# Kernel optimization log

Measured on AMD Instinct MI355X. Metric: run time of the kernel, lower is better.

## Reference

```python
import jax, jax.numpy as jnp
import numpy as np

N = 8_000_000
NUM_MOLS = 200_000

def setup_inputs() -> dict:
    key = jax.random.key(0)
    k1, k2 = jax.random.split(key)
    atoms_x = jax.random.normal(k1, (N, 3), dtype=jnp.float32)
    graph_batch = jnp.sort(jax.random.randint(k2, (N,), 0, NUM_MOLS, dtype=jnp.int64))
    return {"atoms_x": atoms_x, "graph_batch": graph_batch, "num_mols": NUM_MOLS}

def reference(atoms_x, graph_batch, num_mols):
    # Per-molecule mean via single-pass segment reduction (replaces O(N*num_mols) mask loop)
    seg_sum = jax.ops.segment_sum(atoms_x, graph_batch, num_segments=num_mols)          # [M, 3]
    counts = jax.ops.segment_sum(jnp.ones((atoms_x.shape[0],), atoms_x.dtype),
                                 graph_batch, num_segments=num_mols)                    # [M]
    mean = seg_sum / jnp.maximum(counts, 1.0)[:, None]                                  # empty mols -> 0 center
    return atoms_x - mean[graph_batch]
```

## Files before the change

### kernel.cpp

```cpp
#include <hip/hip_runtime.h>


static constexpr int WAVE   = 64;
static constexpr int TPB    = 64;
static constexpr int CPT    = 8;
static constexpr int WCHUNK = WAVE * CPT;
static constexpr int SLOTS  = 96;
static constexpr int NGRP   = WCHUNK / 16;
static constexpr int XGRP   = 216;
static constexpr int IGRP   = 72;

#define LDS_FENCE() asm volatile("s_waitcnt lgkmcnt(0)" ::: "memory")

__device__ void serial_fallback(const float* __restrict__ x,
                                const int* __restrict__ gb,
                                float* __restrict__ out, int n,
                                long long cs, long long ce, int lane) {
  if (lane != 0) return;
  long long i = cs;
  while (i < ce) {
    int id = gb[i];
    long long rs = i; while (rs > 0 && gb[rs - 1] == id) --rs;
    long long re = i; while (re < n && gb[re] == id) ++re;
    float sx = 0.f, sy = 0.f, sz = 0.f;
    for (long long k = rs; k < re; ++k) {
      sx += x[k * 3 + 0]; sy += x[k * 3 + 1]; sz += x[k * 3 + 2];
    }
    float inv = 1.f / (float)(re - rs);
    float mx = sx * inv, my = sy * inv, mz = sz * inv;
    long long we = (re < ce) ? re : ce;
    for (long long k = i; k < we; ++k) {
      out[k * 3 + 0] = x[k * 3 + 0] - mx;
      out[k * 3 + 1] = x[k * 3 + 1] - my;
      out[k * 3 + 2] = x[k * 3 + 2] - mz;
    }
    i = we;
  }
}

__global__ __launch_bounds__(TPB) void fused_center_kernel(
    const float* __restrict__ x, const int* __restrict__ gb,
    float* __restrict__ out, int n) {
  __shared__ alignas(16) char xbuf[NGRP * XGRP];
  __shared__ alignas(16) char ibuf[NGRP * IGRP];
  __shared__ alignas(16) float sums[SLOTS * 4];

  const int lane = threadIdx.x;
  const long long cs = (long long)blockIdx.x * WCHUNK;
  const long long ce = (cs + WCHUNK < (long long)n) ? cs + WCHUNK : (long long)n;

  if (ce - cs < WCHUNK) {
    const int fid = gb[cs];
    const int lid = gb[ce - 1];
    const int span = lid - fid + 1;
    if (span > SLOTS) { serial_fallback(x, gb, out, n, cs, ce, lane); return; }
    for (int s = lane; s < span * 4; s += WAVE) sums[s] = 0.f;
    LDS_FENCE();
    for (long long i = cs + lane; i < ce; i += WAVE) {
      int s = (gb[i] - fid) * 4;
      atomicAdd(&sums[s + 0], x[i * 3 + 0]);
      atomicAdd(&sums[s + 1], x[i * 3 + 1]);
      atomicAdd(&sums[s + 2], x[i * 3 + 2]);
      atomicAdd(&sums[s + 3], 1.f);
    }
    if (cs > 0) {
      float hx = 0.f, hy = 0.f, hz = 0.f, hc = 0.f;
      long long off = 1 + lane;
      for (;;) {
        long long i = cs - off;
        bool m = (i >= 0) && (gb[i] == fid);
        if (m) { hx += x[i*3+0]; hy += x[i*3+1]; hz += x[i*3+2]; hc += 1.f; }
        if (__popcll(__ballot(m)) < WAVE) break;
        off += WAVE;
      }
#pragma unroll
      for (int d = 1; d < 64; d <<= 1) {
        hx += __shfl_xor(hx, d); hy += __shfl_xor(hy, d);
        hz += __shfl_xor(hz, d); hc += __shfl_xor(hc, d);
      }
      if (lane == 0 && hc > 0.f) {
        atomicAdd(&sums[0], hx); atomicAdd(&sums[1], hy);
        atomicAdd(&sums[2], hz); atomicAdd(&sums[3], hc);
      }
    }
    LDS_FENCE();
    for (int s = lane; s < span; s += WAVE) {
      float c = sums[s * 4 + 3];
      if (c > 0.f) {
        float inv = 1.f / c;
        sums[s*4+0] *= inv; sums[s*4+1] *= inv; sums[s*4+2] *= inv;
      }
    }
    LDS_FENCE();
    for (long long i = cs + lane; i < ce; i += WAVE) {
      int s = (gb[i] - fid) * 4;
      out[i * 3 + 0] = x[i * 3 + 0] - sums[s + 0];
      out[i * 3 + 1] = x[i * 3 + 1] - sums[s + 1];
      out[i * 3 + 2] = x[i * 3 + 2] - sums[s + 2];
    }
    return;
  }

  float4 xr[6];
  const float4* xv = reinterpret_cast<const float4*>(x + cs * 3);
#pragma unroll
  for (int j = 0; j < 6; ++j) xr[j] = xv[j * WAVE + lane];
  int4 gr[2];
  const int4* gv = reinterpret_cast<const int4*>(gb + cs);
#pragma unroll
  for (int j = 0; j < 2; ++j) gr[j] = gv[j * WAVE + lane];

#pragma unroll
  for (int j = 0; j < 6; ++j) {
    int i = j * WAVE + lane;
    int k0 = 2 * i, k1 = 2 * i + 1;
    *reinterpret_cast<float2*>(xbuf + (k0 / 24) * XGRP + (k0 % 24) * 8) =
        make_float2(xr[j].x, xr[j].y);
    *reinterpret_cast<float2*>(xbuf + (k1 / 24) * XGRP + (k1 % 24) * 8) =
        make_float2(xr[j].z, xr[j].w);
  }
#pragma unroll
  for (int j = 0; j < 2; ++j) {
    int i = j * WAVE + lane;
    int k0 = 2 * i, k1 = 2 * i + 1;
    *reinterpret_cast<int2*>(ibuf + (k0 / 8) * IGRP + (k0 % 8) * 8) =
        make_int2(gr[j].x, gr[j].y);
    *reinterpret_cast<int2*>(ibuf + (k1 / 8) * IGRP + (k1 % 8) * 8) =
        make_int2(gr[j].z, gr[j].w);
  }
  {
    float4 z = make_float4(0.f, 0.f, 0.f, 0.f);
    reinterpret_cast<float4*>(sums)[lane] = z;
    if (lane < SLOTS - WAVE) reinterpret_cast<float4*>(sums)[WAVE + lane] = z;
  }
  LDS_FENCE();

  int idk[CPT];
  const int a0 = lane * CPT;
#pragma unroll
  for (int j = 0; j < CPT; ++j) {
    int a = a0 + j;
    idk[j] = *reinterpret_cast<const int*>(ibuf + (a / 16) * IGRP + (a % 16) * 4);
  }
  const int fid = __shfl(idk[0], 0);
  const int lid = __shfl(idk[CPT - 1], WAVE - 1);
  const int span = lid - fid + 1;
  if (span > SLOTS) { serial_fallback(x, gb, out, n, cs, ce, lane); return; }

  {
    int cur = idk[0];
    float sx = 0.f, sy = 0.f, sz = 0.f, sc = 0.f;
#pragma unroll
    for (int j = 0; j < CPT; ++j) {
      if (idk[j] != cur) {
        int s = (cur - fid) * 4;
        atomicAdd(&sums[s + 0], sx); atomicAdd(&sums[s + 1], sy);
        atomicAdd(&sums[s + 2], sz); atomicAdd(&sums[s + 3], sc);
        cur = idk[j]; sx = sy = sz = sc = 0.f;
      }
      int a = a0 + j;
      const char* p = xbuf + (a / 16) * XGRP + (a % 16) * 12;
      sx += *reinterpret_cast<const float*>(p + 0);
      sy += *reinterpret_cast<const float*>(p + 4);
      sz += *reinterpret_cast<const float*>(p + 8);
      sc += 1.f;
    }
    int s = (cur - fid) * 4;
    atomicAdd(&sums[s + 0], sx); atomicAdd(&sums[s + 1], sy);
    atomicAdd(&sums[s + 2], sz); atomicAdd(&sums[s + 3], sc);
  }

  if (cs > 0) {
    float hx = 0.f, hy = 0.f, hz = 0.f, hc = 0.f;
    long long off = 1 + lane;
    for (;;) {
      long long i = cs - off;
      bool m = (i >= 0) && (gb[i] == fid);
      if (m) { hx += x[i*3+0]; hy += x[i*3+1]; hz += x[i*3+2]; hc += 1.f; }
      if (__popcll(__ballot(m)) < WAVE) break;
      off += WAVE;
    }
#pragma unroll
    for (int d = 1; d < 64; d <<= 1) {
      hx += __shfl_xor(hx, d); hy += __shfl_xor(hy, d);
      hz += __shfl_xor(hz, d); hc += __shfl_xor(hc, d);
    }
    if (lane == 0 && hc > 0.f) {
      atomicAdd(&sums[0], hx); atomicAdd(&sums[1], hy);
      atomicAdd(&sums[2], hz); atomicAdd(&sums[3], hc);
    }
  }
  if (ce < (long long)n) {
    float hx = 0.f, hy = 0.f, hz = 0.f, hc = 0.f;
    long long off = (long long)lane;
    for (;;) {
      long long i = ce + off;
      bool m = (i < (long long)n) && (gb[i] == lid);
      if (m) { hx += x[i*3+0]; hy += x[i*3+1]; hz += x[i*3+2]; hc += 1.f; }
      if (__popcll(__ballot(m)) < WAVE) break;
      off += WAVE;
    }
#pragma unroll
    for (int d = 1; d < 64; d <<= 1) {
      hx += __shfl_xor(hx, d); hy += __shfl_xor(hy, d);
      hz += __shfl_xor(hz, d); hc += __shfl_xor(hc, d);
    }
    if (lane == 0 && hc > 0.f) {
      int s = (lid - fid) * 4;
      atomicAdd(&sums[s + 0], hx); atomicAdd(&sums[s + 1], hy);
      atomicAdd(&sums[s + 2], hz); atomicAdd(&sums[s + 3], hc);
    }
  }
  LDS_FENCE();

  for (int s = lane; s < span; s += WAVE) {
    float c = sums[s * 4 + 3];
    if (c > 0.f) {
      float inv = 1.f / c;
      sums[s*4+0] *= inv; sums[s*4+1] *= inv; sums[s*4+2] *= inv;
    }
  }
  LDS_FENCE();

  float4* ov = reinterpret_cast<float4*>(out + cs * 3);
#pragma unroll
  for (int j = 0; j < 6; ++j) {
    int i = j * WAVE + lane;
    int e = 4 * i;
    float4 o;
#pragma unroll
    for (int c = 0; c < 4; ++c) {
      int ee = e + c;
      int atom = (int)(((unsigned)ee * 0xAAABu) >> 17);
      int comp = ee - atom * 3;
      int id = *reinterpret_cast<const int*>(
          ibuf + (atom / 16) * IGRP + (atom % 16) * 4);
      float m = sums[(id - fid) * 4 + comp];
      float v = (c == 0) ? xr[j].x : (c == 1) ? xr[j].y
              : (c == 2) ? xr[j].z : xr[j].w;
      if (c == 0) o.x = v - m;
      else if (c == 1) o.y = v - m;
      else if (c == 2) o.z = v - m;
      else o.w = v - m;
    }
    ov[i] = o;
  }
}

extern "C" void kernel_launch(void* const* d_in, const int* in_sizes, int n_in,
                              void* d_out, int out_size, void* d_ws, size_t ws_size,
                              hipStream_t stream) {
  const float* x = (const float*)d_in[0];
  const int* gb = (const int*)d_in[1];
  float* out = (float*)d_out;
  const int n = in_sizes[0] / 3;

  int blocks = (int)(((long long)n + WCHUNK - 1) / WCHUNK);
  fused_center_kernel<<<blocks, TPB, 0, stream>>>(x, gb, out, n);
}
```

Before: 60.97 us.

## Pack four waves per block and rework LDS layout to scatter per-atom means

Each block now runs four independent waves, each handling its own 512-atom chunk with private LDS buffers, which cuts the block count by four. The LDS staging uses a padded word layout (26 words per 24) so each lane reads its 8 atoms as contiguous float2s without bank conflicts. The output phase no longer looks up a segment id and mean for every element: each lane writes its atoms' means back into the x staging buffer, and the coalesced store reads them from there. SLOTS drops from 96 to 64, so chunks spanning more molecules fall back to the slow serial path more often; with this test data that should be rare.

```diff
diff --git a/kernel.cpp b/kernel.cpp
--- a/kernel.cpp
+++ b/kernel.cpp
@@ -2,15 +2,17 @@
 
 
 static constexpr int WAVE   = 64;
-static constexpr int TPB    = 64;
+static constexpr int WPB    = 4;
+static constexpr int TPB    = WAVE * WPB;
 static constexpr int CPT    = 8;
 static constexpr int WCHUNK = WAVE * CPT;
-static constexpr int SLOTS  = 96;
-static constexpr int NGRP   = WCHUNK / 16;
-static constexpr int XGRP   = 216;
-static constexpr int IGRP   = 72;
+static constexpr int SLOTS  = 64;
+static constexpr int XWORDS = (WCHUNK * 3 / 24) * 26;
+static constexpr int IWORDS = WCHUNK + WCHUNK / 8;
 
 #define LDS_FENCE() asm volatile("s_waitcnt lgkmcnt(0)" ::: "memory")
+
+__device__ __forceinline__ int xw(int k) { return (k / 24) * 26 + (k % 24); }
 
 __device__ void serial_fallback(const float* __restrict__ x,
                                 const int* __restrict__ gb,
@@ -41,12 +43,18 @@
 __global__ __launch_bounds__(TPB) void fused_center_kernel(
     const float* __restrict__ x, const int* __restrict__ gb,
     float* __restrict__ out, int n) {
-  __shared__ alignas(16) char xbuf[NGRP * XGRP];
-  __shared__ alignas(16) char ibuf[NGRP * IGRP];
-  __shared__ alignas(16) float sums[SLOTS * 4];
-
-  const int lane = threadIdx.x;
-  const long long cs = (long long)blockIdx.x * WCHUNK;
+  __shared__ float xbuf_all[WPB][XWORDS];
+  __shared__ int   ibuf_all[WPB][IWORDS];
+  __shared__ float sums_all[WPB][SLOTS*4];
+
+  const int w = threadIdx.x >> 6;
+  const int lane = threadIdx.x & 63;
+  float* xbuf = xbuf_all[w];
+  int*   ibuf = ibuf_all[w];
+  float* sums = sums_all[w];
+
+  const long long cs = ((long long)blockIdx.x * WPB + w) * WCHUNK;
+  if (cs >= (long long)n) return;
   const long long ce = (cs + WCHUNK < (long long)n) ? cs + WCHUNK : (long long)n;
 
   if (ce - cs < WCHUNK) {
@@ -110,42 +118,36 @@
 #pragma unroll
   for (int j = 0; j < 2; ++j) gr[j] = gv[j * WAVE + lane];
 
-#pragma unroll
-  for (int j = 0; j < 6; ++j) {
-    int i = j * WAVE + lane;
-    int k0 = 2 * i, k1 = 2 * i + 1;
-    *reinterpret_cast<float2*>(xbuf + (k0 / 24) * XGRP + (k0 % 24) * 8) =
-        make_float2(xr[j].x, xr[j].y);
-    *reinterpret_cast<float2*>(xbuf + (k1 / 24) * XGRP + (k1 % 24) * 8) =
-        make_float2(xr[j].z, xr[j].w);
-  }
-#pragma unroll
-  for (int j = 0; j < 2; ++j) {
-    int i = j * WAVE + lane;
-    int k0 = 2 * i, k1 = 2 * i + 1;
-    *reinterpret_cast<int2*>(ibuf + (k0 / 8) * IGRP + (k0 % 8) * 8) =
-        make_int2(gr[j].x, gr[j].y);
-    *reinterpret_cast<int2*>(ibuf + (k1 / 8) * IGRP + (k1 % 8) * 8) =
-        make_int2(gr[j].z, gr[j].w);
-  }
-  {
-    float4 z = make_float4(0.f, 0.f, 0.f, 0.f);
-    reinterpret_cast<float4*>(sums)[lane] = z;
-    if (lane < SLOTS - WAVE) reinterpret_cast<float4*>(sums)[WAVE + lane] = z;
-  }
-  LDS_FENCE();
-
-  int idk[CPT];
-  const int a0 = lane * CPT;
-#pragma unroll
-  for (int j = 0; j < CPT; ++j) {
-    int a = a0 + j;
-    idk[j] = *reinterpret_cast<const int*>(ibuf + (a / 16) * IGRP + (a % 16) * 4);
-  }
-  const int fid = __shfl(idk[0], 0);
-  const int lid = __shfl(idk[CPT - 1], WAVE - 1);
+  const int fid = __shfl(gr[0].x, 0);
+  const int lid = __shfl(gr[1].w, WAVE - 1);
   const int span = lid - fid + 1;
   if (span > SLOTS) { serial_fallback(x, gb, out, n, cs, ce, lane); return; }
+
+#pragma unroll
+  for (int j = 0; j < 6; ++j) {
+    int k = (j * WAVE + lane) * 4;
+    *reinterpret_cast<float2*>(&xbuf[xw(k)])     = make_float2(xr[j].x, xr[j].y);
+    *reinterpret_cast<float2*>(&xbuf[xw(k + 2)]) = make_float2(xr[j].z, xr[j].w);
+  }
+#pragma unroll
+  for (int j = 0; j < 2; ++j) {
+    int k = (j * WAVE + lane) * 4;
+    int b = k + (k >> 3);
+    ibuf[b + 0] = gr[j].x; ibuf[b + 1] = gr[j].y;
+    ibuf[b + 2] = gr[j].z; ibuf[b + 3] = gr[j].w;
+  }
+  reinterpret_cast<float4*>(sums)[lane] = make_float4(0.f, 0.f, 0.f, 0.f);
+  LDS_FENCE();
+
+  int idk[CPT];
+#pragma unroll
+  for (int j = 0; j < CPT; ++j) idk[j] = ibuf[9 * lane + j];
+  float f[CPT * 3];
+#pragma unroll
+  for (int j = 0; j < 12; ++j) {
+    float2 t = *reinterpret_cast<float2*>(&xbuf[26 * lane + 2 * j]);
+    f[2*j] = t.x; f[2*j+1] = t.y;
+  }
 
   {
     int cur = idk[0];
@@ -158,12 +160,7 @@
         atomicAdd(&sums[s + 2], sz); atomicAdd(&sums[s + 3], sc);
         cur = idk[j]; sx = sy = sz = sc = 0.f;
       }
-      int a = a0 + j;
-      const char* p = xbuf + (a / 16) * XGRP + (a % 16) * 12;
-      sx += *reinterpret_cast<const float*>(p + 0);
-      sy += *reinterpret_cast<const float*>(p + 4);
-      sz += *reinterpret_cast<const float*>(p + 8);
-      sc += 1.f;
+      sx += f[j * 3 + 0]; sy += f[j * 3 + 1]; sz += f[j * 3 + 2]; sc += 1.f;
     }
     int s = (cur - fid) * 4;
     atomicAdd(&sums[s + 0], sx); atomicAdd(&sums[s + 1], sy);
@@ -213,37 +210,42 @@
   }
   LDS_FENCE();
 
-  for (int s = lane; s < span; s += WAVE) {
-    float c = sums[s * 4 + 3];
+  if (lane < span) {
+    float c = sums[lane * 4 + 3];
     if (c > 0.f) {
       float inv = 1.f / c;
-      sums[s*4+0] *= inv; sums[s*4+1] *= inv; sums[s*4+2] *= inv;
-    }
+      sums[lane*4+0] *= inv; sums[lane*4+1] *= inv; sums[lane*4+2] *= inv;
+    }
+  }
+  LDS_FENCE();
+
+  {
+    float marr[CPT * 3];
+    int prev = idk[0];
+    float4 mv = *reinterpret_cast<float4*>(&sums[(prev - fid) * 4]);
+#pragma unroll
+    for (int j = 0; j < CPT; ++j) {
+      if (idk[j] != prev) {
+        prev = idk[j];
+        mv = *reinterpret_cast<float4*>(&sums[(prev - fid) * 4]);
+      }
+      marr[3*j+0] = mv.x; marr[3*j+1] = mv.y; marr[3*j+2] = mv.z;
+    }
+#pragma unroll
+    for (int j = 0; j < 12; ++j)
+      *reinterpret_cast<float2*>(&xbuf[26 * lane + 2 * j]) =
+          make_float2(marr[2*j], marr[2*j+1]);
   }
   LDS_FENCE();
 
   float4* ov = reinterpret_cast<float4*>(out + cs * 3);
 #pragma unroll
   for (int j = 0; j < 6; ++j) {
-    int i = j * WAVE + lane;
-    int e = 4 * i;
-    float4 o;
-#pragma unroll
-    for (int c = 0; c < 4; ++c) {
-      int ee = e + c;
-      int atom = (int)(((unsigned)ee * 0xAAABu) >> 17);
-      int comp = ee - atom * 3;
-      int id = *reinterpret_cast<const int*>(
-          ibuf + (atom / 16) * IGRP + (atom % 16) * 4);
-      float m = sums[(id - fid) * 4 + comp];
-      float v = (c == 0) ? xr[j].x : (c == 1) ? xr[j].y
-              : (c == 2) ? xr[j].z : xr[j].w;
-      if (c == 0) o.x = v - m;
-      else if (c == 1) o.y = v - m;
-      else if (c == 2) o.z = v - m;
-      else o.w = v - m;
-    }
-    ov[i] = o;
+    int k = (j * WAVE + lane) * 4;
+    float2 a = *reinterpret_cast<float2*>(&xbuf[xw(k)]);
+    float2 b = *reinterpret_cast<float2*>(&xbuf[xw(k + 2)]);
+    ov[j * WAVE + lane] = make_float4(xr[j].x - a.x, xr[j].y - a.y,
+                                      xr[j].z - b.x, xr[j].w - b.y);
   }
 }
 
@@ -255,6 +257,7 @@
   float* out = (float*)d_out;
   const int n = in_sizes[0] / 3;
 
-  int blocks = (int)(((long long)n + WCHUNK - 1) / WCHUNK);
+  long long nchunks = ((long long)n + WCHUNK - 1) / WCHUNK;
+  int blocks = (int)((nchunks + WPB - 1) / WPB);
   fused_center_kernel<<<blocks, TPB, 0, stream>>>(x, gb, out, n);
 }
```

Result: slower. 62.65 us (+2.8%).
